# Optimization experiments

Measured on AMD Instinct MI355X. Metric: run time of the kernel, lower is better.

Reference implementation:

```python
import jax, jax.numpy as jnp
import numpy as np

NUM_LAYERS = 4
EPS = 1e-8


def setup_inputs() -> dict:
    key = jax.random.key(0)
    ks = jax.random.split(key, 7)
    N, D, H = 8192, 1024, 4096
    return {
        "x": jax.random.normal(ks[0], (N, D), jnp.float32),
        "fc1_W": jax.random.normal(ks[1], (H, D), jnp.float32) * 0.02,
        "fc1_b": jax.random.normal(ks[2], (H,), jnp.float32) * 0.02,
        "fc2_W": jax.random.normal(ks[3], (D, H), jnp.float32) * 0.02,
        "fc2_b": jax.random.normal(ks[4], (D,), jnp.float32) * 0.02,
        "comp_W": jax.random.normal(ks[5], (NUM_LAYERS + 1, D, D), jnp.float32) * 0.03,
        "comp_b": jax.random.normal(ks[6], (NUM_LAYERS + 1, D), jnp.float32) * 0.03,
    }


def _block(x, fc1_W, fc1_b, fc2_W, fc2_b):
    # fc2(dropout(fc1(x))) in eval mode; relu is defined but never applied
    h = x @ fc1_W.T + fc1_b
    return h @ fc2_W.T + fc2_b


def _compute_loss(z, W, b):
    # out = Linear(z); per-row cosine_similarity(out_i.unsqueeze(1), out_i.unsqueeze(0))
    # reduces broadcast dim 1 -> vector c[j] = out[j]*sum(out) / max(|out[j]|*sqrt(y)*||out||, eps)
    # which torch broadcasts into constant rows of a [y,y] matrix; the
    # abs-diff accumulation over batch rows is then rank-1.
    out = z @ W.T + b                                # [N, y]
    y = out.shape[-1]
    S = out.sum(-1, keepdims=True)                   # [N, 1]
    n2 = jnp.sqrt((out * out).sum(-1, keepdims=True))  # [N, 1] row norms
    n1 = jnp.abs(out) * jnp.sqrt(jnp.asarray(y, out.dtype))  # [N, y]
    c = out * S / jnp.maximum(n1 * n2, EPS)          # [N, y]
    D = jnp.abs(c[1:] - c[:-1]).sum(0)               # [y]
    return jnp.broadcast_to(D, (y, y))               # [y, y]


def reference(x, fc1_W, fc1_b, fc2_W, fc2_b, comp_W, comp_b):
    inv = _block(x, fc1_W, fc1_b, fc2_W, fc2_b)
    loss = _compute_loss(inv, comp_W[0], comp_b[0])
    nxt = x - inv
    inv_total = inv
    for i in range(1, NUM_LAYERS + 1):
        inv_new = _block(nxt, fc1_W, fc1_b, fc2_W, fc2_b)
        inv_total = inv_total + inv_new
        loss = loss + _compute_loss(inv_new, comp_W[i], comp_b[i])
        nxt = nxt - inv_new
    return inv_total, nxt, loss
```

## Files before the change

### kernel.cpp

```cpp
#include <hip/hip_runtime.h>
#include <hip/hip_bf16.h>


#define NR 8192
#define DD 1024
#define HH 4096
#define NL 5
#define MSZ (DD * DD)

using bf16 = __hip_bfloat16;
typedef __attribute__((ext_vector_type(8))) short bf16x8;
typedef __attribute__((ext_vector_type(4))) float f32x4;


__device__ __forceinline__ void cvt4(const float* __restrict__ in, bf16* __restrict__ out, int i) {
  float4 v = ((const float4*)in)[i];
  union { bf16 b[4]; uint2 u; } u;
  u.b[0] = __float2bfloat16(v.x); u.b[1] = __float2bfloat16(v.y);
  u.b[2] = __float2bfloat16(v.z); u.b[3] = __float2bfloat16(v.w);
  ((uint2*)out)[i] = u.u;
}

#define NX4 (NR * DD / 4)
#define NF4 (DD * HH / 4)
#define NC4 (NL * MSZ / 4)
#define NS4 ((NL * DD + 2 * NL * NR) / 4)
#define NE4 (DD)

__global__ void prep_kernel(const float* __restrict__ x, const float* __restrict__ fc2_W,
                            const float* __restrict__ comp_W,
                            bf16* __restrict__ x_bf, bf16* __restrict__ fc2_bf,
                            bf16* __restrict__ compW_bf,
                            float* __restrict__ stats, float* __restrict__ ebuf) {
  int i = blockIdx.x * 256 + threadIdx.x;
  const int stride = gridDim.x * 256;
  const int total = NX4 + NF4 + NC4 + NS4 + NE4;
  const float4 z4 = {0.f, 0.f, 0.f, 0.f};
  for (; i < total; i += stride) {
    if (i < NX4) cvt4(x, x_bf, i);
    else if (i < NX4 + NF4) cvt4(fc2_W, fc2_bf, i - NX4);
    else if (i < NX4 + NF4 + NC4) cvt4(comp_W, compW_bf, i - NX4 - NF4);
    else if (i < NX4 + NF4 + NC4 + NS4) ((float4*)stats)[i - NX4 - NF4 - NC4] = z4;
    else ((float4*)ebuf)[i - NX4 - NF4 - NC4 - NS4] = z4;
  }
}

__global__ void transpose_cvt_kernel(const float* __restrict__ in, bf16* __restrict__ out) {
  __shared__ bf16 tile[64][74];
  int c0 = blockIdx.x * 64;
  int r0 = blockIdx.y * 64;
  int col = threadIdx.x & 63;
  int row4 = threadIdx.x >> 6;
  #pragma unroll
  for (int j = 0; j < 16; ++j) {
    int r = row4 * 16 + j;
    tile[r][col] = __float2bfloat16(in[(size_t)(r0 + r) * DD + c0 + col]);
  }
  __syncthreads();
  #pragma unroll
  for (int j = 0; j < 16; ++j) {
    int r = row4 * 16 + j;
    out[(size_t)(c0 + r) * HH + r0 + col] = tile[col][r];
  }
}

__global__ void cvec_kernel(const float* __restrict__ fc1_b, const float* __restrict__ fc2_W,
                            const float* __restrict__ fc2_b, float* __restrict__ c) {
  int j = blockIdx.x;
  float s = 0.f;
  for (int k = threadIdx.x; k < HH; k += 256) s += fc1_b[k] * fc2_W[(size_t)j * HH + k];
  for (int o = 32; o; o >>= 1) s += __shfl_down(s, o);
  __shared__ float red[4];
  if ((threadIdx.x & 63) == 0) red[threadIdx.x >> 6] = s;
  __syncthreads();
  if (threadIdx.x == 0) c[j] = red[0] + red[1] + red[2] + red[3] + fc2_b[j];
}

__global__ void mbuild_kernel(const float* __restrict__ Cp,
                              bf16* __restrict__ M, bf16* __restrict__ T, bf16* __restrict__ Tt) {
  __shared__ float tile[64][65];
  int n0 = blockIdx.x * 64, m0 = blockIdx.y * 64;
  int tn = threadIdx.x & 63, tm4 = threadIdx.x >> 6;
  #pragma unroll
  for (int j = 0; j < 16; ++j) {
    int m = tm4 * 16 + j;
    size_t idx = (size_t)(m0 + m) * DD + n0 + tn;
    float v = Cp[idx] + Cp[MSZ + idx] + Cp[2 * MSZ + idx] + Cp[3 * MSZ + idx];
    tile[m][tn] = v;
    float d = ((m0 + m) == (n0 + tn)) ? 1.f : 0.f;
    M[idx] = __float2bfloat16(v);
    T[idx] = __float2bfloat16(d - v);
  }
  __syncthreads();
  #pragma unroll
  for (int j = 0; j < 16; ++j) {
    int r = tm4 * 16 + j;
    float v = tile[tn][r];
    size_t idx = (size_t)(n0 + r) * DD + m0 + tn;
    float d = ((n0 + r) == (m0 + tn)) ? 1.f : 0.f;
    Tt[idx] = __float2bfloat16(d - v);
  }
}

__global__ void gemv4_kernel(const float* __restrict__ c, const bf16* __restrict__ Pw,
                             float* __restrict__ ebuf) {
  const int z = blockIdx.y;
  const int j = blockIdx.x * 256 + threadIdx.x;
  const bf16* P = Pw + (size_t)z * MSZ + j;
  const int k0 = blockIdx.z * 256;
  float s = 0.f;
  #pragma unroll 8
  for (int k = k0; k < k0 + 256; ++k) s += c[k] * __bfloat162float(P[(size_t)k * DD]);
  atomicAdd(&ebuf[z * DD + j], s);
}

__global__ void biasall_kernel(const float* __restrict__ cvec, const float* __restrict__ ebuf,
                               const float* __restrict__ comp_W, const float* __restrict__ comp_b,
                               float* __restrict__ biasall) {
  int z = blockIdx.y, j = blockIdx.x;
  if (z == 0) {
    if (threadIdx.x == 0)
      biasall[j] = cvec[j] + ebuf[j] + ebuf[DD + j] + ebuf[2 * DD + j] + ebuf[3 * DD + j];
    return;
  }
  int i = z - 1;
  const float* e = (i == 0) ? cvec : ebuf + (size_t)(i - 1) * DD;
  const float* wr = comp_W + (size_t)i * MSZ + (size_t)j * DD;
  float s = 0.f;
  for (int k = threadIdx.x; k < DD; k += 256) s += e[k] * wr[k];
  for (int o = 32; o; o >>= 1) s += __shfl_down(s, o);
  __shared__ float red[4];
  if ((threadIdx.x & 63) == 0) red[threadIdx.x >> 6] = s;
  __syncthreads();
  if (threadIdx.x == 0)
    biasall[(size_t)z * DD + j] = red[0] + red[1] + red[2] + red[3] + comp_b[(size_t)i * DD + j];
}


__device__ __forceinline__ void async16(const bf16* g, bf16* l) {
  __builtin_amdgcn_global_load_lds(
      (const __attribute__((address_space(1))) void*)g,
      (__attribute__((address_space(3))) void*)l, 16, 0, 0);
}

__device__ __forceinline__ void gemm_core_async(
    const bf16* __restrict__ A, const bf16* __restrict__ B,
    int kBeg, int kEnd, int lda, int ldb, int bm, int bn,
    bf16* As, bf16* Bs, f32x4 acc[4][4])
{
  const int tid  = threadIdx.x;
  const int lane = tid & 63;
  const int wave = tid >> 6;
  const int wm = (wave & 1) * 64;
  const int wn = (wave >> 1) * 64;
  const int lr = lane >> 3;
  const int lcol = ((lane & 7) ^ lr) * 8;
  const bf16* gA = A + (size_t)(bm + wave * 32 + lr) * lda + lcol;
  const bf16* gB = B + (size_t)(bn + wave * 32 + lr) * ldb + lcol;
  bf16* lA = As + wave * 32 * 64;
  bf16* lB = Bs + wave * 32 * 64;

  for (int k0 = kBeg; k0 < kEnd; k0 += 64) {
    #pragma unroll
    for (int it = 0; it < 4; ++it) {
      async16(gA + (size_t)(it * 8) * lda + k0, lA + it * 8 * 64);
      async16(gB + (size_t)(it * 8) * ldb + k0, lB + it * 8 * 64);
    }
    __syncthreads();
    #pragma unroll
    for (int ks = 0; ks < 2; ++ks) {
      bf16x8 av[4], bv[4];
      #pragma unroll
      for (int i = 0; i < 4; ++i) {
        const int rr = i * 16 + (lane & 15);
        const int cc = ((ks * 4 + (lane >> 4)) ^ (lane & 7)) * 8;
        av[i] = *(const bf16x8*)(As + (wm + rr) * 64 + cc);
        bv[i] = *(const bf16x8*)(Bs + (wn + rr) * 64 + cc);
      }
      #pragma unroll
      for (int i = 0; i < 4; ++i)
        #pragma unroll
        for (int j = 0; j < 4; ++j)
          acc[i][j] = __builtin_amdgcn_mfma_f32_16x16x32_bf16(av[i], bv[j], acc[i][j], 0, 0, 0);
    }
    __syncthreads();
  }
}

__device__ __forceinline__ void gemm_core64(
    const bf16* __restrict__ A, const bf16* __restrict__ B,
    int kBeg, int kEnd, int lda, int ldb, int bm, int bn,
    bf16* As, bf16* Bs, f32x4 acc[2][2])
{
  const int tid  = threadIdx.x;
  const int lane = tid & 63;
  const int wave = tid >> 6;
  const int wm = (wave & 1) * 32;
  const int wn = (wave >> 1) * 32;
  const int lr = lane >> 3;
  const int lcol = ((lane & 7) ^ lr) * 8;
  const bf16* gA = A + (size_t)(bm + wave * 16 + lr) * lda + lcol;
  const bf16* gB = B + (size_t)(bn + wave * 16 + lr) * ldb + lcol;
  bf16* lA = As + wave * 16 * 64;
  bf16* lB = Bs + wave * 16 * 64;

  for (int k0 = kBeg; k0 < kEnd; k0 += 64) {
    #pragma unroll
    for (int it = 0; it < 2; ++it) {
      async16(gA + (size_t)(it * 8) * lda + k0, lA + it * 8 * 64);
      async16(gB + (size_t)(it * 8) * ldb + k0, lB + it * 8 * 64);
    }
    __syncthreads();
    #pragma unroll
    for (int ks = 0; ks < 2; ++ks) {
      bf16x8 av[2], bv[2];
      #pragma unroll
      for (int i = 0; i < 2; ++i) {
        const int rr = i * 16 + (lane & 15);
        const int cc = ((ks * 4 + (lane >> 4)) ^ (lane & 7)) * 8;
        av[i] = *(const bf16x8*)(As + (wm + rr) * 64 + cc);
        bv[i] = *(const bf16x8*)(Bs + (wn + rr) * 64 + cc);
      }
      #pragma unroll
      for (int i = 0; i < 2; ++i)
        #pragma unroll
        for (int j = 0; j < 2; ++j)
          acc[i][j] = __builtin_amdgcn_mfma_f32_16x16x32_bf16(av[i], bv[j], acc[i][j], 0, 0, 0);
    }
    __syncthreads();
  }
}

#define GEMM_PROLOGUE \
  alignas(16) __shared__ bf16 As[128 * 64]; \
  alignas(16) __shared__ bf16 Bs[128 * 64]; \
  f32x4 acc[4][4] = {}; \
  const int lane = threadIdx.x & 63; \
  const int wm = ((threadIdx.x >> 6) & 1) * 64; \
  const int wn = ((threadIdx.x >> 6) >> 1) * 64;

#define GEMM_PROLOGUE64 \
  alignas(16) __shared__ bf16 As[64 * 64]; \
  alignas(16) __shared__ bf16 Bs[64 * 64]; \
  f32x4 acc[2][2] = {}; \
  const int lane = threadIdx.x & 63; \
  const int wm = ((threadIdx.x >> 6) & 1) * 32; \
  const int wn = ((threadIdx.x >> 6) >> 1) * 32;

__global__ __launch_bounds__(256, 4)
void gemm_splitk64(const bf16* __restrict__ A, const bf16* __restrict__ B, float* __restrict__ Cp) {
  GEMM_PROLOGUE64
  const int bm = blockIdx.y * 64, bn = blockIdx.x * 64;
  const int kb = blockIdx.z * (HH / 4);
  gemm_core64(A, B, kb, kb + HH / 4, HH, HH, bm, bn, As, Bs, acc);
  float* C = Cp + (size_t)blockIdx.z * MSZ;
  #pragma unroll
  for (int i = 0; i < 2; ++i)
    #pragma unroll
    for (int j = 0; j < 2; ++j) {
      const int col = bn + wn + j * 16 + (lane & 15);
      #pragma unroll
      for (int r = 0; r < 4; ++r) {
        const int row = bm + wm + i * 16 + (lane >> 4) * 4 + r;
        C[(size_t)row * DD + col] = acc[i][j][r];
      }
    }
}

__global__ __launch_bounds__(256, 4)
void gemm_dual64(const bf16* __restrict__ A, const bf16* __restrict__ B,
                 bf16* __restrict__ Ct, bf16* __restrict__ Cn) {
  GEMM_PROLOGUE64
  const int bm = blockIdx.y * 64, bn = blockIdx.x * 64;
  gemm_core64(A, B, 0, DD, DD, DD, bm, bn, As, Bs, acc);
  #pragma unroll
  for (int i = 0; i < 2; ++i)
    #pragma unroll
    for (int j = 0; j < 2; ++j) {
      const int col = bn + wn + j * 16 + (lane & 15);
      const int row0 = bm + wm + i * 16 + (lane >> 4) * 4;
      union { bf16 b[4]; uint2 u; } pk;
      #pragma unroll
      for (int r = 0; r < 4; ++r) {
        bf16 v = __float2bfloat16(acc[i][j][r]);
        pk.b[r] = v;
        Cn[(size_t)(row0 + r) * DD + col] = v;
      }
      *(uint2*)(&Ct[(size_t)col * DD + row0]) = pk.u;
    }
}

__global__ __launch_bounds__(256, 4)
void gemm_b64(const bf16* __restrict__ A0, long astr, const bf16* __restrict__ B0, long bstr,
              bf16* __restrict__ C0, long cstr) {
  GEMM_PROLOGUE64
  const int z = blockIdx.z;
  const bf16* A = A0 + (size_t)z * astr;
  const bf16* B = B0 + (size_t)z * bstr;
  bf16* C = C0 + (size_t)z * cstr;
  const int bm = blockIdx.y * 64, bn = blockIdx.x * 64;
  gemm_core64(A, B, 0, DD, DD, DD, bm, bn, As, Bs, acc);
  #pragma unroll
  for (int i = 0; i < 2; ++i)
    #pragma unroll
    for (int j = 0; j < 2; ++j) {
      const int col = bn + wn + j * 16 + (lane & 15);
      #pragma unroll
      for (int r = 0; r < 4; ++r) {
        const int row = bm + wm + i * 16 + (lane >> 4) * 4 + r;
        C[(size_t)row * DD + col] = __float2bfloat16(acc[i][j][r]);
      }
    }
}

__global__ __launch_bounds__(256, 4)
void gemm_t5_64(const bf16* __restrict__ A, const bf16* __restrict__ B,
                const bf16* __restrict__ Pw, bf16* __restrict__ Dl, bf16* __restrict__ Bbig0) {
  GEMM_PROLOGUE64
  const int bm = blockIdx.y * 64, bn = blockIdx.x * 64;
  gemm_core64(A, B, 0, DD, DD, DD, bm, bn, As, Bs, acc);
  #pragma unroll
  for (int i = 0; i < 2; ++i)
    #pragma unroll
    for (int j = 0; j < 2; ++j) {
      const int col = bn + wn + j * 16 + (lane & 15);
      const int row0 = bm + wm + i * 16 + (lane >> 4) * 4;
      union { bf16 b[4]; uint2 u; } pk;
      #pragma unroll
      for (int r = 0; r < 4; ++r) {
        const size_t idx = (size_t)(row0 + r) * DD + col;
        const float t1 = __bfloat162float(Pw[idx]);
        const float t2 = __bfloat162float(Pw[MSZ + idx]);
        const float t3 = __bfloat162float(Pw[2 * MSZ + idx]);
        const float t4 = __bfloat162float(Pw[3 * MSZ + idx]);
        const float t5 = acc[i][j][r];
        Dl[idx]           = __float2bfloat16(t1 - t2);
        Dl[MSZ + idx]     = __float2bfloat16(t2 - t3);
        Dl[2 * MSZ + idx] = __float2bfloat16(t3 - t4);
        Dl[3 * MSZ + idx] = __float2bfloat16(t4 - t5);
        pk.b[r] = __float2bfloat16((((row0 + r) == col) ? 1.f : 0.f) - t5);
      }
      *(uint2*)(&Bbig0[(size_t)col * DD + row0]) = pk.u;
    }
}

__global__ __launch_bounds__(256, 2)
void gemm_main(const bf16* __restrict__ A, const bf16* __restrict__ Bb,
               const float* __restrict__ biasall, const bf16* __restrict__ xb,
               float* __restrict__ invtot, float* __restrict__ nxtf,
               unsigned long long* __restrict__ sgn,
               float* __restrict__ Srow, float* __restrict__ Qrow) {
  GEMM_PROLOGUE
  const int bm = blockIdx.y * 128, bn = blockIdx.x * 128;
  gemm_core_async(A, Bb + (size_t)(bn >> 10) * MSZ, 0, DD, DD, DD, bm, bn & (DD - 1), As, Bs, acc);

  if (bn < DD) {
    #pragma unroll
    for (int i = 0; i < 4; ++i)
      #pragma unroll
      for (int j = 0; j < 4; ++j) {
        const int col = bn + wn + j * 16 + (lane & 15);
        const float bj = biasall[col];
        #pragma unroll
        for (int r = 0; r < 4; ++r) {
          const int row = bm + wm + i * 16 + (lane >> 4) * 4 + r;
          const float v = acc[i][j][r] + bj;
          const size_t idx = (size_t)row * DD + col;
          invtot[idx] = v;
          nxtf[idx] = __bfloat162float(xb[idx]) - v;
        }
      }
  } else {
    const int z = (bn >> 10) - 1;
    const int rb = bm >> 7;
    const int cb = (bn & (DD - 1)) >> 7;
    const int wave = threadIdx.x >> 6;
    unsigned long long keep = 0ULL;
    float sv[4][4] = {}, qv[4][4] = {};
    #pragma unroll
    for (int i = 0; i < 4; ++i)
      #pragma unroll
      for (int j = 0; j < 4; ++j) {
        const int colg = bn + wn + j * 16 + (lane & 15);
        const float bj = biasall[colg];
        #pragma unroll
        for (int r = 0; r < 4; ++r) {
          const float v = acc[i][j][r] + bj;
          const unsigned long long bal = __ballot(v < 0.f);
          if (lane == i * 16 + j * 4 + r) keep = bal;
          sv[i][r] += v;
          qv[i][r] += v * v;
        }
      }
    const size_t wbase = ((((size_t)z * 64 + rb) * 8 + cb) * 4 + wave) * 64;
    sgn[wbase + lane] = keep;
    #pragma unroll
    for (int i = 0; i < 4; ++i)
      #pragma unroll
      for (int r = 0; r < 4; ++r) {
        float s = sv[i][r], q = qv[i][r];
        #pragma unroll
        for (int off = 1; off < 16; off <<= 1) { s += __shfl_xor(s, off); q += __shfl_xor(q, off); }
        if ((lane & 15) == 0) {
          const int row = bm + wm + i * 16 + (lane >> 4) * 4 + r;
          atomicAdd(&Srow[(size_t)z * NR + row], s);
          atomicAdd(&Qrow[(size_t)z * NR + row], q);
        }
      }
  }
}


__global__ void losssign_kernel(const unsigned long long* __restrict__ sgn,
                                const float* __restrict__ Srow, const float* __restrict__ Qrow,
                                float* __restrict__ Dtot) {
  const int z = blockIdx.y;
  const int cg = blockIdx.x;
  const int n0 = blockIdx.z * 1024;
  __shared__ float rsh[1025];
  const float* S = Srow + (size_t)z * NR;
  const float* Q = Qrow + (size_t)z * NR;
  for (int t = threadIdx.x; t < 1025; t += 256) {
    int n = n0 + t; if (n > NR - 1) n = NR - 1;
    rsh[t] = S[n] * rsqrtf(Q[n]) * 0.03125f;
  }
  __syncthreads();
  const int c = threadIdx.x & 63;
  const int q = threadIdx.x >> 6;
  const int col = cg * 64 + c;
  const int cb = col >> 7;
  const int wsel = (col >> 6) & 1;
  const int jf = (col >> 4) & 3;
  const int c15 = col & 15;
  const size_t zbase = (size_t)z * 64 * 8 * 4 * 64;
  const int ns = n0 + q * 256;
  int ne = ns + 256; if (ne > NR - 1) ne = NR - 1;

  auto cval = [&](int n) -> float {
    const int rbk = n >> 7, nl = n & 127;
    const int wave = (nl >> 6) | (wsel << 1);
    const int i = (nl >> 4) & 3, rg = (nl >> 2) & 3, r = nl & 3;
    const size_t widx = zbase + ((((size_t)rbk * 8 + cb) * 4 + wave) * 64)
                      + i * 16 + jf * 4 + r;
    const unsigned long long wv = sgn[widx];
    const float rv = rsh[n - n0];
    return ((wv >> (rg * 16 + c15)) & 1ULL) ? -rv : rv;
  };

  float d = 0.f;
  float cprev = cval(ns);
  for (int n = ns + 1; n <= ne; ++n) {
    const float cn = cval(n);
    d += fabsf(cn - cprev);
    cprev = cn;
  }
  atomicAdd(&Dtot[z * DD + col], d);
}

__global__ void writeloss_kernel(const float* __restrict__ Dtot, float* __restrict__ out) {
  int idx = blockIdx.x * 256 + threadIdx.x;
  int j = idx & (DD - 1);
  out[idx] = Dtot[j] + Dtot[DD + j] + Dtot[2 * DD + j] + Dtot[3 * DD + j] + Dtot[4 * DD + j];
}


extern "C" void kernel_launch(void* const* d_in, const int* in_sizes, int n_in,
                              void* d_out, int out_size, void* d_ws, size_t ws_size,
                              hipStream_t stream) {
  const float* x      = (const float*)d_in[0];
  const float* fc1_W  = (const float*)d_in[1];
  const float* fc1_b  = (const float*)d_in[2];
  const float* fc2_W  = (const float*)d_in[3];
  const float* fc2_b  = (const float*)d_in[4];
  const float* comp_W = (const float*)d_in[5];
  const float* comp_b = (const float*)d_in[6];

  float* invtot  = (float*)d_out;
  float* nxtf    = invtot + (size_t)NR * DD;
  float* lossout = invtot + (size_t)2 * NR * DD;

  char* w = (char*)d_ws;
  auto alloc = [&](size_t bytes) { char* p = w; w += (bytes + 255) & ~(size_t)255; return p; };
  bf16* x_bf     = (bf16*)alloc((size_t)NR * DD * 2);
  bf16* fc1T_bf  = (bf16*)alloc((size_t)DD * HH * 2);
  bf16* fc2_bf   = (bf16*)alloc((size_t)DD * HH * 2);
  bf16* compW_bf = (bf16*)alloc((size_t)NL * MSZ * 2);
  bf16* Dbank    = (bf16*)alloc((size_t)5 * MSZ * 2);
  bf16* M_bf = Dbank;
  bf16* Dl   = Dbank + MSZ;
  bf16* Tt_buf   = (bf16*)alloc((size_t)2 * MSZ * 2);
  bf16* Pw       = (bf16*)alloc((size_t)4 * MSZ * 2);
  bf16* Bbig     = (bf16*)alloc((size_t)6 * MSZ * 2);
  unsigned long long* sgn = (unsigned long long*)alloc((size_t)NL * 64 * 8 * 4 * 64 * 8);
  float* Cp      = (float*)alloc((size_t)4 * MSZ * 4);
  float* cvec    = (float*)alloc(DD * 4);
  float* ebuf    = (float*)alloc((size_t)4 * DD * 4);
  float* biasall = (float*)alloc((size_t)6 * DD * 4);
  float* stats   = (float*)alloc((size_t)(NL * DD + 2 * NL * NR) * 4);
  float* Dtot = stats;
  float* Srow = stats + NL * DD;
  float* Qrow = Srow + (size_t)NL * NR;
  (void)ws_size; (void)in_sizes; (void)n_in; (void)out_size;

  prep_kernel<<<2048, 256, 0, stream>>>(x, fc2_W, comp_W, x_bf, fc2_bf, compW_bf, stats, ebuf);
  transpose_cvt_kernel<<<dim3(DD / 64, HH / 64), 256, 0, stream>>>(fc1_W, fc1T_bf);
  cvec_kernel<<<DD, 256, 0, stream>>>(fc1_b, fc2_W, fc2_b, cvec);

  gemm_splitk64<<<dim3(16, 16, 4), 256, 0, stream>>>(fc1T_bf, fc2_bf, Cp);
  mbuild_kernel<<<dim3(16, 16), 256, 0, stream>>>(Cp, M_bf, Pw, Tt_buf);
  gemm_dual64<<<dim3(16, 16), 256, 0, stream>>>(Pw, Tt_buf, Tt_buf + MSZ, Pw + MSZ);
  gemm_b64<<<dim3(16, 16, 2), 256, 0, stream>>>(Pw + MSZ, 0, Tt_buf, MSZ, Pw + 2 * MSZ, MSZ);
  gemm_t5_64<<<dim3(16, 16), 256, 0, stream>>>(Pw + 3 * MSZ, Tt_buf, Pw, Dl, Bbig);
  gemv4_kernel<<<dim3(4, 4, 4), 256, 0, stream>>>(cvec, Pw, ebuf);
  biasall_kernel<<<dim3(DD, 6), 256, 0, stream>>>(cvec, ebuf, comp_W, comp_b, biasall);
  gemm_b64<<<dim3(16, 16, NL), 256, 0, stream>>>(compW_bf, MSZ, Dbank, MSZ, Bbig + MSZ, MSZ);

  gemm_main<<<dim3(6 * DD / 128, NR / 128), 256, 0, stream>>>(
      x_bf, Bbig, biasall, x_bf, invtot, nxtf, sgn, Srow, Qrow);

  losssign_kernel<<<dim3(16, NL, 8), 256, 0, stream>>>(sgn, Srow, Qrow, Dtot);
  writeloss_kernel<<<MSZ / 256, 256, 0, stream>>>(Dtot, lossout);
}
```

Baseline: 483.1 us.

## Replace main GEMM with 256x256 double-buffered 8-wave pipelined kernel

The 128x128 single-buffered main GEMM becomes a 256x256 tile kernel with 512 threads. It double-buffers LDS (128KB) and overlaps async global-to-LDS staging with MFMA work through fine-grained waitcnt, barriers and setprio. The sign-bit buffer is laid out row-major per 64-column group, which simplifies indexing in the loss-sign kernel. The larger tiles raise data reuse and hide load latency, at the cost of heavy LDS use that caps occupancy and more register pressure from the 8x4 accumulators.

```diff
diff --git a/kernel.cpp b/kernel.cpp
--- a/kernel.cpp
+++ b/kernel.cpp
@@ -141,50 +141,6 @@
   __builtin_amdgcn_global_load_lds(
       (const __attribute__((address_space(1))) void*)g,
       (__attribute__((address_space(3))) void*)l, 16, 0, 0);
-}
-
-__device__ __forceinline__ void gemm_core_async(
-    const bf16* __restrict__ A, const bf16* __restrict__ B,
-    int kBeg, int kEnd, int lda, int ldb, int bm, int bn,
-    bf16* As, bf16* Bs, f32x4 acc[4][4])
-{
-  const int tid  = threadIdx.x;
-  const int lane = tid & 63;
-  const int wave = tid >> 6;
-  const int wm = (wave & 1) * 64;
-  const int wn = (wave >> 1) * 64;
-  const int lr = lane >> 3;
-  const int lcol = ((lane & 7) ^ lr) * 8;
-  const bf16* gA = A + (size_t)(bm + wave * 32 + lr) * lda + lcol;
-  const bf16* gB = B + (size_t)(bn + wave * 32 + lr) * ldb + lcol;
-  bf16* lA = As + wave * 32 * 64;
-  bf16* lB = Bs + wave * 32 * 64;
-
-  for (int k0 = kBeg; k0 < kEnd; k0 += 64) {
-    #pragma unroll
-    for (int it = 0; it < 4; ++it) {
-      async16(gA + (size_t)(it * 8) * lda + k0, lA + it * 8 * 64);
-      async16(gB + (size_t)(it * 8) * ldb + k0, lB + it * 8 * 64);
-    }
-    __syncthreads();
-    #pragma unroll
-    for (int ks = 0; ks < 2; ++ks) {
-      bf16x8 av[4], bv[4];
-      #pragma unroll
-      for (int i = 0; i < 4; ++i) {
-        const int rr = i * 16 + (lane & 15);
-        const int cc = ((ks * 4 + (lane >> 4)) ^ (lane & 7)) * 8;
-        av[i] = *(const bf16x8*)(As + (wm + rr) * 64 + cc);
-        bv[i] = *(const bf16x8*)(Bs + (wn + rr) * 64 + cc);
-      }
-      #pragma unroll
-      for (int i = 0; i < 4; ++i)
-        #pragma unroll
-        for (int j = 0; j < 4; ++j)
-          acc[i][j] = __builtin_amdgcn_mfma_f32_16x16x32_bf16(av[i], bv[j], acc[i][j], 0, 0, 0);
-    }
-    __syncthreads();
-  }
 }
 
 __device__ __forceinline__ void gemm_core64(
@@ -231,14 +187,6 @@
   }
 }
 
-#define GEMM_PROLOGUE \
-  alignas(16) __shared__ bf16 As[128 * 64]; \
-  alignas(16) __shared__ bf16 Bs[128 * 64]; \
-  f32x4 acc[4][4] = {}; \
-  const int lane = threadIdx.x & 63; \
-  const int wm = ((threadIdx.x >> 6) & 1) * 64; \
-  const int wn = ((threadIdx.x >> 6) >> 1) * 64;
-
 #define GEMM_PROLOGUE64 \
   alignas(16) __shared__ bf16 As[64 * 64]; \
   alignas(16) __shared__ bf16 Bs[64 * 64]; \
@@ -344,26 +292,112 @@
     }
 }
 
-__global__ __launch_bounds__(256, 2)
-void gemm_main(const bf16* __restrict__ A, const bf16* __restrict__ Bb,
-               const float* __restrict__ biasall, const bf16* __restrict__ xb,
-               float* __restrict__ invtot, float* __restrict__ nxtf,
-               unsigned long long* __restrict__ sgn,
-               float* __restrict__ Srow, float* __restrict__ Qrow) {
-  GEMM_PROLOGUE
-  const int bm = blockIdx.y * 128, bn = blockIdx.x * 128;
-  gemm_core_async(A, Bb + (size_t)(bn >> 10) * MSZ, 0, DD, DD, DD, bm, bn & (DD - 1), As, Bs, acc);
-
-  if (bn < DD) {
-    #pragma unroll
-    for (int i = 0; i < 4; ++i)
+
+__global__ __launch_bounds__(512, 2)
+void gemm_main256(const bf16* __restrict__ A, const bf16* __restrict__ Bb,
+                  const float* __restrict__ biasall, const bf16* __restrict__ xb,
+                  float* __restrict__ invtot, float* __restrict__ nxtf,
+                  unsigned long long* __restrict__ sgn,
+                  float* __restrict__ Srow, float* __restrict__ Qrow) {
+  __shared__ bf16 Ls[65536];
+  const int tid  = threadIdx.x;
+  const int lane = tid & 63;
+  const int w    = tid >> 6;
+  const int wr   = w >> 2, wc = w & 3;
+  const int gbn  = blockIdx.x * 256;
+  const int bm   = blockIdx.y * 256;
+  const int zm   = gbn >> 10;
+  const int cbase = gbn & (DD - 1);
+  const bf16* Bz = Bb + (size_t)zm * MSZ;
+
+  f32x4 acc[8][4] = {};
+
+  const int lr  = lane >> 3;
+  const int lc  = ((lane & 7) ^ lr) * 8;
+  const int l15 = lane & 15;
+  const int cc0 = (((lane >> 4)    ) ^ (lane & 7)) * 8;
+  const int cc1 = (((lane >> 4) + 4) ^ (lane & 7)) * 8;
+
+  auto ldsHalf = [&](int buf, int mat, int half) -> bf16* {
+    return Ls + (((buf << 2) | (mat << 1) | half) << 13);
+  };
+  auto stageHalf = [&](int buf, int mat, int half, int k0) {
+    const bf16* g = (mat == 0)
+      ? A  + (size_t)(bm    + half * 128 + w * 16 + lr) * DD + k0 + lc
+      : Bz + (size_t)(cbase + half * 128 + w * 16 + lr) * DD + k0 + lc;
+    bf16* d = ldsHalf(buf, mat, half) + w * 1024;
+    async16(g, d);
+    async16(g + (size_t)8 * DD, d + 512);
+  };
+
+  stageHalf(0, 0, 0, 0); stageHalf(0, 0, 1, 0);
+  stageHalf(0, 1, 0, 0); stageHalf(0, 1, 1, 0);
+  asm volatile("s_waitcnt vmcnt(0)" ::: "memory");
+  __builtin_amdgcn_sched_barrier(0);
+  __builtin_amdgcn_s_barrier();
+  __builtin_amdgcn_sched_barrier(0);
+
+  #pragma unroll 2
+  for (int t = 0; t < 16; ++t) {
+    const int p = t & 1;
+    const bf16* Ah = ldsHalf(p, 0, wr);
+    const bf16* Bh = ldsHalf(p, 1, wc >> 1);
+    const int brl = (wc & 1) * 64;
+    const int k1 = (t + 1) * 64;
+    #pragma unroll
+    for (int ph = 0; ph < 4; ++ph) {
+      const int qm = ph & 1, qn = ph >> 1;
+      if (ph == 0) {
+        if (t < 15) stageHalf(p ^ 1, 0, 0, k1);
+        __builtin_amdgcn_sched_barrier(0);
+        if (t < 15) { asm volatile("s_waitcnt vmcnt(2)" ::: "memory"); }
+        else        { asm volatile("s_waitcnt vmcnt(0)" ::: "memory"); }
+        __builtin_amdgcn_sched_barrier(0);
+        __builtin_amdgcn_s_barrier();
+        __builtin_amdgcn_sched_barrier(0);
+      } else {
+        if (t < 15) stageHalf(p ^ 1, ph >> 1, ph & 1, k1);
+      }
+      bf16x8 av[4][2], bv[2][2];
+      #pragma unroll
+      for (int i2 = 0; i2 < 4; ++i2) {
+        const bf16* ap = Ah + (qm * 64 + i2 * 16 + l15) * 64;
+        av[i2][0] = *(const bf16x8*)(ap + cc0);
+        av[i2][1] = *(const bf16x8*)(ap + cc1);
+      }
+      #pragma unroll
+      for (int j2 = 0; j2 < 2; ++j2) {
+        const bf16* bp = Bh + (brl + qn * 32 + j2 * 16 + l15) * 64;
+        bv[j2][0] = *(const bf16x8*)(bp + cc0);
+        bv[j2][1] = *(const bf16x8*)(bp + cc1);
+      }
+      __builtin_amdgcn_s_setprio(1);
+      #pragma unroll
+      for (int i2 = 0; i2 < 4; ++i2)
+        #pragma unroll
+        for (int j2 = 0; j2 < 2; ++j2) {
+          acc[qm * 4 + i2][qn * 2 + j2] = __builtin_amdgcn_mfma_f32_16x16x32_bf16(
+              av[i2][0], bv[j2][0], acc[qm * 4 + i2][qn * 2 + j2], 0, 0, 0);
+          acc[qm * 4 + i2][qn * 2 + j2] = __builtin_amdgcn_mfma_f32_16x16x32_bf16(
+              av[i2][1], bv[j2][1], acc[qm * 4 + i2][qn * 2 + j2], 0, 0, 0);
+        }
+      __builtin_amdgcn_s_setprio(0);
+      __builtin_amdgcn_sched_barrier(0);
+      __builtin_amdgcn_s_barrier();
+      __builtin_amdgcn_sched_barrier(0);
+    }
+  }
+
+  if (zm == 0) {
+    #pragma unroll
+    for (int i = 0; i < 8; ++i)
       #pragma unroll
       for (int j = 0; j < 4; ++j) {
-        const int col = bn + wn + j * 16 + (lane & 15);
+        const int col = cbase + wc * 64 + j * 16 + l15;
         const float bj = biasall[col];
         #pragma unroll
         for (int r = 0; r < 4; ++r) {
-          const int row = bm + wm + i * 16 + (lane >> 4) * 4 + r;
+          const int row = bm + wr * 128 + i * 16 + (lane >> 4) * 4 + r;
           const float v = acc[i][j][r] + bj;
           const size_t idx = (size_t)row * DD + col;
           invtot[idx] = v;
@@ -371,42 +405,48 @@
         }
       }
   } else {
-    const int z = (bn >> 10) - 1;
-    const int rb = bm >> 7;
-    const int cb = (bn & (DD - 1)) >> 7;
-    const int wave = threadIdx.x >> 6;
-    unsigned long long keep = 0ULL;
-    float sv[4][4] = {}, qv[4][4] = {};
-    #pragma unroll
-    for (int i = 0; i < 4; ++i)
-      #pragma unroll
-      for (int j = 0; j < 4; ++j) {
-        const int colg = bn + wn + j * 16 + (lane & 15);
-        const float bj = biasall[colg];
+    const int z = zm - 1;
+    const int cg = (cbase >> 6) + wc;
+    unsigned long long keep0 = 0ULL, keep1 = 0ULL;
+    #pragma unroll
+    for (int i = 0; i < 8; ++i) {
+      float sv[4] = {0.f, 0.f, 0.f, 0.f}, qv[4] = {0.f, 0.f, 0.f, 0.f};
+      #pragma unroll
+      for (int r = 0; r < 4; ++r) {
+        unsigned long long bal[4];
         #pragma unroll
-        for (int r = 0; r < 4; ++r) {
+        for (int j = 0; j < 4; ++j) {
+          const float bj = biasall[gbn + wc * 64 + j * 16 + l15];
           const float v = acc[i][j][r] + bj;
-          const unsigned long long bal = __ballot(v < 0.f);
-          if (lane == i * 16 + j * 4 + r) keep = bal;
-          sv[i][r] += v;
-          qv[i][r] += v * v;
+          bal[j] = __ballot(v < 0.f);
+          sv[r] += v; qv[r] += v * v;
         }
-      }
-    const size_t wbase = ((((size_t)z * 64 + rb) * 8 + cb) * 4 + wave) * 64;
-    sgn[wbase + lane] = keep;
-    #pragma unroll
-    for (int i = 0; i < 4; ++i)
+        #pragma unroll
+        for (int rg = 0; rg < 4; ++rg) {
+          const unsigned long long wv =
+              (((bal[0] >> (rg * 16)) & 0xFFFFULL)      ) |
+              (((bal[1] >> (rg * 16)) & 0xFFFFULL) << 16) |
+              (((bal[2] >> (rg * 16)) & 0xFFFFULL) << 32) |
+              (((bal[3] >> (rg * 16)) & 0xFFFFULL) << 48);
+          const int tl = i * 8 + rg * 2 + (r >> 1);
+          if (lane == tl) { if (r & 1) keep1 = wv; else keep0 = wv; }
+        }
+      }
       #pragma unroll
       for (int r = 0; r < 4; ++r) {
-        float s = sv[i][r], q = qv[i][r];
+        float s = sv[r], q = qv[r];
         #pragma unroll
         for (int off = 1; off < 16; off <<= 1) { s += __shfl_xor(s, off); q += __shfl_xor(q, off); }
-        if ((lane & 15) == 0) {
-          const int row = bm + wm + i * 16 + (lane >> 4) * 4 + r;
+        if (l15 == 0) {
+          const int row = bm + wr * 128 + i * 16 + (lane >> 4) * 4 + r;
           atomicAdd(&Srow[(size_t)z * NR + row], s);
           atomicAdd(&Qrow[(size_t)z * NR + row], q);
         }
       }
+    }
+    const int row0 = bm + wr * 128 + lane * 2;
+    sgn[(((size_t)z * NR + row0) << 4) + cg] = keep0;
+    sgn[(((size_t)z * NR + row0 + 1) << 4) + cg] = keep1;
   }
 }
 
@@ -428,23 +468,13 @@
   const int c = threadIdx.x & 63;
   const int q = threadIdx.x >> 6;
   const int col = cg * 64 + c;
-  const int cb = col >> 7;
-  const int wsel = (col >> 6) & 1;
-  const int jf = (col >> 4) & 3;
-  const int c15 = col & 15;
-  const size_t zbase = (size_t)z * 64 * 8 * 4 * 64;
   const int ns = n0 + q * 256;
   int ne = ns + 256; if (ne > NR - 1) ne = NR - 1;
 
   auto cval = [&](int n) -> float {
-    const int rbk = n >> 7, nl = n & 127;
-    const int wave = (nl >> 6) | (wsel << 1);
-    const int i = (nl >> 4) & 3, rg = (nl >> 2) & 3, r = nl & 3;
-    const size_t widx = zbase + ((((size_t)rbk * 8 + cb) * 4 + wave) * 64)
-                      + i * 16 + jf * 4 + r;
-    const unsigned long long wv = sgn[widx];
+    const unsigned long long wv = sgn[(((size_t)z * NR + n) << 4) + cg];
     const float rv = rsh[n - n0];
-    return ((wv >> (rg * 16 + c15)) & 1ULL) ? -rv : rv;
+    return ((wv >> c) & 1ULL) ? -rv : rv;
   };
 
   float d = 0.f;
@@ -491,7 +521,7 @@
   bf16* Tt_buf   = (bf16*)alloc((size_t)2 * MSZ * 2);
   bf16* Pw       = (bf16*)alloc((size_t)4 * MSZ * 2);
   bf16* Bbig     = (bf16*)alloc((size_t)6 * MSZ * 2);
-  unsigned long long* sgn = (unsigned long long*)alloc((size_t)NL * 64 * 8 * 4 * 64 * 8);
+  unsigned long long* sgn = (unsigned long long*)alloc((size_t)NL * NR * 16 * 8);
   float* Cp      = (float*)alloc((size_t)4 * MSZ * 4);
   float* cvec    = (float*)alloc(DD * 4);
   float* ebuf    = (float*)alloc((size_t)4 * DD * 4);
@@ -515,7 +545,7 @@
   biasall_kernel<<<dim3(DD, 6), 256, 0, stream>>>(cvec, ebuf, comp_W, comp_b, biasall);
   gemm_b64<<<dim3(16, 16, NL), 256, 0, stream>>>(compW_bf, MSZ, Dbank, MSZ, Bbig + MSZ, MSZ);
 
-  gemm_main<<<dim3(6 * DD / 128, NR / 128), 256, 0, stream>>>(
+  gemm_main256<<<dim3(6 * DD / 256, NR / 256), 512, 0, stream>>>(
       x_bf, Bbig, biasall, x_bf, invtot, nxtf, sgn, Srow, Qrow);
 
   losssign_kernel<<<dim3(16, NL, 8), 256, 0, stream>>>(sgn, Srow, Qrow, Dtot);
```

Result: no change. 484.7 us (+0.3%).
